# Performance work log

Measured on AMD Instinct MI355X. Metric: run time of the kernel, lower is better.

## Reference

```python
import jax, jax.numpy as jnp
import numpy as np

PH, PW = 14, 14          # pool_size
SCALE = 1.0              # scale_factor


def setup_inputs() -> dict:
    key = jax.random.key(0)
    k1, k2, k3, k4, k5 = jax.random.split(key, 5)
    H = W = 128
    C = 512
    N = 1000
    img = jax.random.normal(k1, (1, H, W, C), dtype=jnp.float32)
    # valid boxes: x1,y1 in [0,96), width/height deltas in [1,32) -> max coord 126 < 128
    x1 = jax.random.randint(k2, (N,), 0, 96)
    y1 = jax.random.randint(k3, (N,), 0, 96)
    x2 = x1 + jax.random.randint(k4, (N,), 1, 32)
    y2 = y1 + jax.random.randint(k5, (N,), 1, 32)
    rois = jnp.stack([x1, y1, x2, y2], axis=1).astype(jnp.int32)
    return {"img": img, "rois": rois}


def _pool_one(fmap, roi):
    """Crop fmap[y1:y2+1, x1:x2+1] and bilinear-resize to (PH, PW).

    Matches legacy tf.image.resize_images (bilinear, align_corners=False):
    src = dst * (in_size / out_size), edge-clamped.
    fmap: [H, W, C]; roi: (x1, y1, x2, y2) int32.
    """
    x0, y0 = roi[0], roi[1]
    in_w = roi[2] - roi[0] + 1   # w + 1 in the original
    in_h = roi[3] - roi[1] + 1   # h + 1 in the original
    sy = jnp.arange(PH, dtype=jnp.float32) * (in_h.astype(jnp.float32) / PH)
    sx = jnp.arange(PW, dtype=jnp.float32) * (in_w.astype(jnp.float32) / PW)
    yt = jnp.floor(sy).astype(jnp.int32)
    xt = jnp.floor(sx).astype(jnp.int32)
    yb = jnp.minimum(yt + 1, in_h - 1)
    xr = jnp.minimum(xt + 1, in_w - 1)
    wy = (sy - yt.astype(jnp.float32))[:, None, None]   # [PH,1,1]
    wx = (sx - xt.astype(jnp.float32))[None, :, None]   # [1,PW,1]
    rt, rb = y0 + yt, y0 + yb
    cl, cr = x0 + xt, x0 + xr
    v00 = fmap[rt[:, None], cl[None, :]]   # [PH,PW,C]
    v01 = fmap[rt[:, None], cr[None, :]]
    v10 = fmap[rb[:, None], cl[None, :]]
    v11 = fmap[rb[:, None], cr[None, :]]
    top = v00 + wx * (v01 - v00)
    bot = v10 + wx * (v11 - v10)
    return top + wy * (bot - top)


def reference(img, rois):
    # rois_norm = int32(rois * scale_factor)  (floor for non-negative coords)
    rois_n = (rois.astype(jnp.float32) * SCALE).astype(jnp.int32)
    fmap = img[0]   # batch size 1 feature map [H,W,C]
    out = jax.vmap(lambda r: _pool_one(fmap, r))(rois_n)   # [N, PH, PW, C]
    return out
```

## Files before the change

kernel.cpp:

```cpp
#include <hip/hip_runtime.h>

#define PH 14
#define PW 14
#define CC 512
#define IW 128
#define C4G (CC / 4)

typedef float f32x4 __attribute__((ext_vector_type(4)));

__global__ __launch_bounds__(256) void roi_pool_kernel(
    const float* __restrict__ img, const int* __restrict__ rois,
    float* __restrict__ out, int npix, int swizzle) {
  int w = threadIdx.x >> 6;
  int wid;
  if (swizzle) {
    int bid = blockIdx.x;
    int x   = bid & 7;
    int seq = bid >> 3;
    int rg  = seq / 49;
    int k   = seq % 49;
    int r   = rg * 8 + x;
    wid = r * (PH * PW) + k * 4 + w;
  } else {
    wid = blockIdx.x * 4 + w;
  }
  if (wid >= npix) return;
  int pid = __builtin_amdgcn_readfirstlane(wid);
  int lane = threadIdx.x & 63;

  int px = pid % PW;
  int tmp = pid / PW;
  int py = tmp % PH;
  int n = tmp / PH;

  int x0 = rois[n * 4 + 0];
  int y0 = rois[n * 4 + 1];
  int x1 = rois[n * 4 + 2];
  int y1 = rois[n * 4 + 3];
  int in_w = x1 - x0 + 1;
  int in_h = y1 - y0 + 1;

  float scale_y = (float)in_h / (float)PH;
  float scale_x = (float)in_w / (float)PW;
  float sy = (float)py * scale_y;
  float sx = (float)px * scale_x;
  int yt = (int)floorf(sy);
  int xt = (int)floorf(sx);
  int yb = min(yt + 1, in_h - 1);
  int xr = min(xt + 1, in_w - 1);
  float wy = sy - (float)yt;
  float wx = sx - (float)xt;

  int rt = y0 + yt, rb = y0 + yb;
  int cl = x0 + xt, cr = x0 + xr;

  const f32x4* __restrict__ imgv = (const f32x4*)img;
  const f32x4* p00 = imgv + (size_t)(rt * IW + cl) * C4G + lane;
  const f32x4* p01 = imgv + (size_t)(rt * IW + cr) * C4G + lane;
  const f32x4* p10 = imgv + (size_t)(rb * IW + cl) * C4G + lane;
  const f32x4* p11 = imgv + (size_t)(rb * IW + cr) * C4G + lane;

  f32x4 a00 = p00[0], b00 = p00[64];
  f32x4 a01 = p01[0], b01 = p01[64];
  f32x4 a10 = p10[0], b10 = p10[64];
  f32x4 a11 = p11[0], b11 = p11[64];

  f32x4 wxv = wx;
  f32x4 wyv = wy;

  f32x4 atop = a00 + wxv * (a01 - a00);
  f32x4 abot = a10 + wxv * (a11 - a10);
  f32x4 ra = atop + wyv * (abot - atop);

  f32x4 btop = b00 + wxv * (b01 - b00);
  f32x4 bbot = b10 + wxv * (b11 - b10);
  f32x4 rbv = btop + wyv * (bbot - btop);

  f32x4* outv = (f32x4*)out + (size_t)pid * C4G + lane;
  __builtin_nontemporal_store(ra, outv);
  __builtin_nontemporal_store(rbv, outv + 64);
}

extern "C" void kernel_launch(void* const* d_in, const int* in_sizes, int n_in,
                              void* d_out, int out_size, void* d_ws, size_t ws_size,
                              hipStream_t stream) {
  const float* img = (const float*)d_in[0];
  const int* rois = (const int*)d_in[1];
  float* out = (float*)d_out;

  int N = in_sizes[1] / 4;
  int npix = N * PH * PW;
  int blocks = (npix + 3) / 4;
  int swizzle = (N % 8 == 0) ? 1 : 0;
  roi_pool_kernel<<<blocks, 256, 0, stream>>>(img, rois, out, npix, swizzle);
}
```

Measured before the change: 457.7 us.

## Sort ROIs by spatial Morton bucket to improve image cache locality

Adds a single-block counting-sort kernel that buckets ROIs by their center position on an 8x8 Morton-ordered grid and writes a permutation. The pooling kernel's block swizzle then maps the eight concurrent ROI slots through this permutation, so neighboring blocks read overlapping image regions and should hit in L2/MALL more often. The cost is an extra kernel launch and a serial prefix sum. The permutation is also strided across the eight XCD slots, so spatially similar ROIs may land on different XCDs, which could work against locality.

```diff
diff --git a/kernel.cpp b/kernel.cpp
--- a/kernel.cpp
+++ b/kernel.cpp
@@ -8,18 +8,51 @@
 
 typedef float f32x4 __attribute__((ext_vector_type(4)));
 
+__global__ __launch_bounds__(256) void roi_sort_kernel(
+    const int* __restrict__ rois, int* __restrict__ perm, int n) {
+  __shared__ int hist[64];
+  __shared__ int base[64];
+  __shared__ int cnt[64];
+  int t = threadIdx.x;
+  if (t < 64) { hist[t] = 0; cnt[t] = 0; }
+  __syncthreads();
+  for (int r = t; r < n; r += 256) {
+    int xc = min((rois[4 * r + 0] + rois[4 * r + 2]) >> 5, 7);
+    int yc = min((rois[4 * r + 1] + rois[4 * r + 3]) >> 5, 7);
+    int key = (xc & 1) | ((yc & 1) << 1) | ((xc & 2) << 1) | ((yc & 2) << 2) |
+              ((xc & 4) << 2) | ((yc & 4) << 3);
+    atomicAdd(&hist[key], 1);
+  }
+  __syncthreads();
+  if (t == 0) {
+    int s = 0;
+    for (int i = 0; i < 64; i++) { base[i] = s; s += hist[i]; }
+  }
+  __syncthreads();
+  for (int r = t; r < n; r += 256) {
+    int xc = min((rois[4 * r + 0] + rois[4 * r + 2]) >> 5, 7);
+    int yc = min((rois[4 * r + 1] + rois[4 * r + 3]) >> 5, 7);
+    int key = (xc & 1) | ((yc & 1) << 1) | ((xc & 2) << 1) | ((yc & 2) << 2) |
+              ((xc & 4) << 2) | ((yc & 4) << 3);
+    int pos = base[key] + atomicAdd(&cnt[key], 1);
+    perm[pos] = r;
+  }
+}
+
 __global__ __launch_bounds__(256) void roi_pool_kernel(
     const float* __restrict__ img, const int* __restrict__ rois,
-    float* __restrict__ out, int npix, int swizzle) {
+    const int* __restrict__ perm, float* __restrict__ out,
+    int npix, int mode, int nroi8) {
   int w = threadIdx.x >> 6;
   int wid;
-  if (swizzle) {
+  if (mode) {
     int bid = blockIdx.x;
     int x   = bid & 7;
     int seq = bid >> 3;
     int rg  = seq / 49;
     int k   = seq % 49;
-    int r   = rg * 8 + x;
+    int r   = (mode == 2) ? perm[x * nroi8 + rg]
+                          : rg * 8 + x;
     wid = r * (PH * PW) + k * 4 + w;
   } else {
     wid = blockIdx.x * 4 + w;
@@ -91,6 +124,15 @@
   int N = in_sizes[1] / 4;
   int npix = N * PH * PW;
   int blocks = (npix + 3) / 4;
-  int swizzle = (N % 8 == 0) ? 1 : 0;
-  roi_pool_kernel<<<blocks, 256, 0, stream>>>(img, rois, out, npix, swizzle);
+
+  int* perm = (int*)d_ws;
+  int mode = 0;
+  if (N > 0 && (N % 8) == 0) {
+    mode = (d_ws != nullptr && ws_size >= (size_t)N * sizeof(int)) ? 2 : 1;
+  }
+  if (mode == 2) {
+    roi_sort_kernel<<<1, 256, 0, stream>>>(rois, perm, N);
+  }
+  roi_pool_kernel<<<blocks, 256, 0, stream>>>(img, rois, perm, out, npix,
+                                              mode, N / 8);
 }
```

After: 423.2 us. -7.5%, faster.
